# Kernel tuning notes

Measured on AMD Instinct MI355X. Metric: run time of the kernel, lower is better.

## Reference

```python
import jax, jax.numpy as jnp
import numpy as np

N = 20000      # nodes
E = 640000     # edges (avg degree 32)
F_X = 256      # node feature dim
F_E = 256      # edge feature dim
D = 2048       # hidden width
D_OUT = 512    # final Linear out_channels
EPS = 1e-5     # torch LayerNorm default eps


def _glorot_like(k, fan_in, fan_out):
    # torch nn.Linear default: U(-1/sqrt(fan_in), 1/sqrt(fan_in))
    lim = (1.0 / fan_in) ** 0.5
    return jax.random.uniform(k, (fan_in, fan_out), minval=-lim, maxval=lim, dtype=jnp.float32)


def setup_inputs() -> dict:
    key = jax.random.key(0)
    ks = jax.random.split(key, 8)
    return {
        "x": jax.random.normal(ks[0], (N, F_X), dtype=jnp.float32),
        "edge_index": jax.random.randint(ks[1], (2, E), 0, N),
        "edge_attr": jax.random.normal(ks[2], (E, F_E), dtype=jnp.float32),
        # u = (u, nb, eb) in the original; unused by this setup (no conv1d/GraphNorm)
        "u_counts": jnp.array([N], dtype=jnp.int32),
        "nb": jnp.zeros((N,), dtype=jnp.int32),
        "eb": jnp.zeros((E,), dtype=jnp.int32),
        # learned params per setup
        "W1": _glorot_like(ks[3], F_X + F_E, D), "b1": jnp.zeros((D,), jnp.float32),
        "W3": _glorot_like(ks[4], D, D),         "b3": jnp.zeros((D,), jnp.float32),
        "ln_g": jnp.ones((D,), jnp.float32),      "ln_b": jnp.zeros((D,), jnp.float32),
        "W6": _glorot_like(ks[5], D + F_X + F_E, D), "b6": jnp.zeros((D,), jnp.float32),
        "W8": _glorot_like(ks[6], D, D_OUT),      "b8": jnp.zeros((D_OUT,), jnp.float32),
    }


def reference(x, edge_index, edge_attr, u_counts, nb, eb,
              W1, b1, W3, b3, ln_g, ln_b, W6, b6, W8, b8):
    # scatter_mean(edge_attr, col, dim=0, dim_size=N)
    col = edge_index[1]
    seg_sum = jax.ops.segment_sum(edge_attr, col, num_segments=N)           # [N, F_E]
    cnt = jax.ops.segment_sum(jnp.ones((edge_attr.shape[0],), edge_attr.dtype),
                              col, num_segments=N)                           # [N]
    agg = seg_sum / jnp.maximum(cnt, 1.0)[:, None]                           # mean; 0 for empty slots

    h0 = jnp.concatenate([agg, x], axis=1)                                   # [N, F_E+F_X]
    # layer 1-2: Linear -> ReLU
    h2 = jax.nn.relu(h0 @ W1 + b1)                                           # [N, D]
    # layer 3-4: Linear -> ReLU
    h4 = jax.nn.relu(h2 @ W3 + b3)                                           # [N, D]
    # layer 5: LayerNorm (affine)
    mu = jnp.mean(h4, axis=-1, keepdims=True)
    var = jnp.var(h4, axis=-1, keepdims=True)
    h5 = (h4 - mu) * jax.lax.rsqrt(var + EPS) * ln_g + ln_b
    # layer 6-7: Linear over concat(h5, merge_in) -> ReLU  (skip connection)
    h7 = jax.nn.relu(jnp.concatenate([h5, h0], axis=1) @ W6 + b6)            # [N, D]
    # layer 8: Linear -> out[-1]
    return h7 @ W8 + b8                                                      # [N, D_OUT]
```

## Files before the change

### kernel.cpp

```cpp
#include <hip/hip_runtime.h>

typedef unsigned short ushort_t;
typedef __attribute__((ext_vector_type(4))) float f32x4;
typedef __attribute__((ext_vector_type(8))) __bf16 bf16x8;
typedef __attribute__((ext_vector_type(8))) unsigned short u16x8;
typedef __attribute__((ext_vector_type(4))) unsigned short u16x4;

__device__ __forceinline__ unsigned short f2bf(float f) {
  union { float f; unsigned int u; } v; v.f = f;
  unsigned int u = v.u;
  u += 0x7fffu + ((u >> 16) & 1u);
  return (unsigned short)(u >> 16);
}

__device__ __forceinline__ float bf2f(unsigned short h) {
  union { unsigned int u; float f; } v; v.u = ((unsigned int)h) << 16;
  return v.f;
}

__device__ __forceinline__ void gload16(ushort_t* lds, const ushort_t* g) {
  __builtin_amdgcn_global_load_lds(
      (const __attribute__((address_space(1))) unsigned int*)g,
      (__attribute__((address_space(3))) unsigned int*)lds, 16, 0, 0);
}

__global__ __launch_bounds__(256)
void transpose_w(const float* __restrict__ in, ushort_t* __restrict__ out, int R, int C) {
  __shared__ float tile[32][33];
  const int t = threadIdx.x;
  const int tx = t & 31, ty = t >> 5;
  const int r0 = blockIdx.x * 32, c0 = blockIdx.y * 32;
#pragma unroll
  for (int i = 0; i < 4; ++i)
    tile[ty + 8 * i][tx] = in[(size_t)(r0 + ty + 8 * i) * C + c0 + tx];
  __syncthreads();
#pragma unroll
  for (int i = 0; i < 4; ++i)
    out[(size_t)(c0 + ty + 8 * i) * R + r0 + tx] = f2bf(tile[tx][ty + 8 * i]);
}

__global__ __launch_bounds__(256)
void count_edges(const int* __restrict__ col, int* __restrict__ cnt, int E) {
  int i = blockIdx.x * 256 + threadIdx.x;
  if (i < E) atomicAdd(&cnt[col[i]], 1);
}

__global__ __launch_bounds__(1024)
void prefix_kernel(const int* __restrict__ cnt, int* __restrict__ start,
                   int* __restrict__ cursor, int N) {
  const int t = threadIdx.x;
  const int chunk = (N + 1023) >> 10;
  const int base = t * chunk;
  int s = 0;
  for (int j = 0; j < chunk; ++j) {
    int i = base + j;
    s += (i < N) ? cnt[i] : 0;
  }
  const int lane = t & 63, wv = t >> 6;
  int scan = s;
#pragma unroll
  for (int o = 1; o < 64; o <<= 1) {
    int up = __shfl_up(scan, o);
    if (lane >= o) scan += up;
  }
  __shared__ int wsum[16];
  if (lane == 63) wsum[wv] = scan;
  __syncthreads();
  if (t == 0) {
    int acc = 0;
#pragma unroll
    for (int i2 = 0; i2 < 16; ++i2) { int v = wsum[i2]; wsum[i2] = acc; acc += v; }
  }
  __syncthreads();
  int run = wsum[wv] + (scan - s);
  for (int j = 0; j < chunk; ++j) {
    int i = base + j;
    if (i < N) {
      start[i] = run; cursor[i] = run;
      run += cnt[i];
    }
  }
}

__global__ __launch_bounds__(256)
void fill_csr(const int* __restrict__ col, int* __restrict__ cursor,
              int* __restrict__ eids, int E) {
  int i = blockIdx.x * 256 + threadIdx.x;
  if (i < E) {
    int p = atomicAdd(&cursor[col[i]], 1);
    eids[p] = i;
  }
}

__global__ __launch_bounds__(256)
void gather_mean(const float* __restrict__ eattr, const int* __restrict__ start,
                 const int* __restrict__ deg, const int* __restrict__ eids,
                 const float* __restrict__ x, ushort_t* __restrict__ hcat, int N) {
  const int row = blockIdx.x;
  const int t = threadIdx.x;
  const int w = t >> 6, l = t & 63;
  const int s = start[row], d = deg[row];
  const float4* ea4 = (const float4*)eattr;
  float4 sum = make_float4(0.f, 0.f, 0.f, 0.f);
  for (int i = w; i < d; i += 4) {
    int e = eids[s + i];
    float4 v = ea4[(size_t)e * 64 + l];
    sum.x += v.x; sum.y += v.y; sum.z += v.z; sum.w += v.w;
  }
  __shared__ float4 part[4][64];
  part[w][l] = sum;
  __syncthreads();
  hcat[(size_t)row * 2560 + 2304 + t] = f2bf(x[(size_t)row * 256 + t]);
  if (w == 0) {
    float4 a = part[0][l], b = part[1][l], c = part[2][l], dd = part[3][l];
    const float inv = 1.f / fmaxf((float)d, 1.f);
    u16x4 o;
    o[0] = f2bf((a.x + b.x + c.x + dd.x) * inv);
    o[1] = f2bf((a.y + b.y + c.y + dd.y) * inv);
    o[2] = f2bf((a.z + b.z + c.z + dd.z) * inv);
    o[3] = f2bf((a.w + b.w + c.w + dd.w) * inv);
    *(u16x4*)(hcat + (size_t)row * 2560 + 2048 + l * 4) = o;
  }
}

__global__ __launch_bounds__(256)
void ln_kernel(ushort_t* __restrict__ hcat, const float* __restrict__ g,
               const float* __restrict__ b) {
  const int row = blockIdx.x;
  const int t = threadIdx.x;
  ushort_t* p = hcat + (size_t)row * 2560 + t * 8;
  u16x8 raw = *(const u16x8*)p;
  float vv[8];
#pragma unroll
  for (int j = 0; j < 8; ++j) vv[j] = bf2f(raw[j]);
  float s = 0.f, ss = 0.f;
#pragma unroll
  for (int j = 0; j < 8; ++j) { s += vv[j]; ss += vv[j] * vv[j]; }
#pragma unroll
  for (int o = 32; o > 0; o >>= 1) {
    s += __shfl_xor(s, o);
    ss += __shfl_xor(ss, o);
  }
  __shared__ float red[8];
  int w = t >> 6, l = t & 63;
  if (l == 0) { red[w] = s; red[4 + w] = ss; }
  __syncthreads();
  s = red[0] + red[1] + red[2] + red[3];
  ss = red[4] + red[5] + red[6] + red[7];
  const float mu = s * (1.f / 2048.f);
  const float var = ss * (1.f / 2048.f) - mu * mu;
  const float rs = rsqrtf(var + 1e-5f);
  float4 g0 = *(const float4*)(g + t * 8);
  float4 g1 = *(const float4*)(g + t * 8 + 4);
  float4 b0 = *(const float4*)(b + t * 8);
  float4 b1 = *(const float4*)(b + t * 8 + 4);
  float gg[8] = {g0.x, g0.y, g0.z, g0.w, g1.x, g1.y, g1.z, g1.w};
  float bb[8] = {b0.x, b0.y, b0.z, b0.w, b1.x, b1.y, b1.z, b1.w};
  u16x8 o8;
#pragma unroll
  for (int j = 0; j < 8; ++j) o8[j] = f2bf((vv[j] - mu) * rs * gg[j] + bb[j]);
  *(u16x8*)p = o8;
}


__device__ __forceinline__ void read_a4(bf16x8 (&dst)[4][2], const char* sb, int bufoff,
                                        int aoff, int slot0, int slot1, int g) {
#pragma unroll
  for (int m = 0; m < 4; ++m) {
    const char* p = sb + bufoff + aoff + (g * 4 + m) * 2048;
    dst[m][0] = *(const bf16x8*)(p + slot0);
    dst[m][1] = *(const bf16x8*)(p + slot1);
  }
}

__device__ __forceinline__ void read_b2(bf16x8 (&dst)[2][2], const char* sb, int bufoff,
                                        int boff, int slot0, int slot1, int g) {
#pragma unroll
  for (int n = 0; n < 2; ++n) {
    const char* p = sb + bufoff + boff + (g * 2 + n) * 2048;
    dst[n][0] = *(const bf16x8*)(p + slot0);
    dst[n][1] = *(const bf16x8*)(p + slot1);
  }
}

__device__ __forceinline__ void mfma_q(f32x4 (&acc)[8][4], const bf16x8 (&a)[4][2],
                                       const bf16x8 (&b)[2][2], int mg, int ng) {
#pragma unroll
  for (int m = 0; m < 4; ++m)
#pragma unroll
    for (int n = 0; n < 2; ++n)
#pragma unroll
      for (int kk = 0; kk < 2; ++kk)
        acc[mg * 4 + m][ng * 2 + n] = __builtin_amdgcn_mfma_f32_16x16x32_bf16(
            a[m][kk], b[n][kk], acc[mg * 4 + m][ng * 2 + n], 0, 0, 0);
}

#define SBAR() do { __builtin_amdgcn_sched_barrier(0); \
                    __builtin_amdgcn_s_barrier(); \
                    __builtin_amdgcn_sched_barrier(0); } while (0)

template <int RELU, int OUTBF>
__global__ __launch_bounds__(512, 2)
void gemm256(const ushort_t* __restrict__ A, int lda,
             const ushort_t* __restrict__ Bt,
             const float* __restrict__ bias,
             void* __restrict__ Cout, int ldc, int M, int K) {
  __shared__ __align__(16) ushort_t smem[65536];
  char* sb = (char*)smem;
  const int t = threadIdx.x;

  const int nct = gridDim.x;
  const int nwg = nct * gridDim.y;
  const int flat = blockIdx.y * nct + blockIdx.x;
  const int xcd = flat & 7, loc = flat >> 3;
  const int q = nwg >> 3, r = nwg & 7;
  const int swz = (xcd < r ? xcd * (q + 1) : r * (q + 1) + (xcd - r) * q) + loc;
  const int row0 = (swz / nct) * 256;
  const int col0 = (swz % nct) * 256;

  const int wid = t >> 6, l = t & 63;
  const int wr = wid >> 2, wc = wid & 3;
  const int lr = l & 15, lk = l >> 4;

  const int srow = t >> 3;
  const int scol = ((t & 7) ^ ((t >> 3) & 7)) << 3;
  const ushort_t* pa[2][2];
  const ushort_t* pb[2][2];
#pragma unroll
  for (int h = 0; h < 2; ++h)
#pragma unroll
    for (int L = 0; L < 2; ++L) {
      int ra = row0 + h * 128 + L * 64 + srow;
      if (ra > M - 1) ra = M - 1;
      pa[h][L] = A + (size_t)ra * lda + scol;
      pb[h][L] = Bt + (size_t)(col0 + h * 128 + L * 64 + srow) * K + scol;
    }
  const int tb = t * 16;

  const int slot0 = ((lk ^ (lr & 7)) << 4);
  const int slot1 = (((4 + lk) ^ (lr & 7)) << 4);
  const int aoff = (wr * 128 + lr) * 128;
  const int boff = 32768 + (wc * 64 + lr) * 128;

  f32x4 acc[8][4] = {};
  bf16x8 af[4][2], af2[4][2], bf[2][2], bf2[2][2];

  const int nk = K >> 6;

  {
    gload16((ushort_t*)(sb + 0 + tb), pa[0][0]);
    gload16((ushort_t*)(sb + 8192 + tb), pa[0][1]);
    gload16((ushort_t*)(sb + 16384 + tb), pa[1][0]);
    gload16((ushort_t*)(sb + 24576 + tb), pa[1][1]);
    gload16((ushort_t*)(sb + 32768 + tb), pb[0][0]);
    gload16((ushort_t*)(sb + 40960 + tb), pb[0][1]);
    gload16((ushort_t*)(sb + 49152 + tb), pb[1][0]);
    gload16((ushort_t*)(sb + 57344 + tb), pb[1][1]);
    const int k1 = (nk > 1) ? 1 : 0;
    gload16((ushort_t*)(sb + 65536 + 32768 + tb), pb[0][0] + (k1 << 6));
    gload16((ushort_t*)(sb + 65536 + 40960 + tb), pb[0][1] + (k1 << 6));
    gload16((ushort_t*)(sb + 65536 + 0 + tb), pa[0][0] + (k1 << 6));
    gload16((ushort_t*)(sb + 65536 + 8192 + tb), pa[0][1] + (k1 << 6));
  }
  asm volatile("s_waitcnt vmcnt(4)" ::: "memory");
  SBAR();

  for (int k = 0; k < nk; ++k) {
    const int cur = (k & 1) << 16, nxt = cur ^ 65536;
    const int kc1 = ((k + 1 < nk) ? k + 1 : nk - 1) << 6;
    const int kc2 = ((k + 2 < nk) ? k + 2 : nk - 1) << 6;

    read_a4(af, sb, cur, aoff, slot0, slot1, 0);
    read_b2(bf, sb, cur, boff, slot0, slot1, 0);
    gload16((ushort_t*)(sb + nxt + 16384 + tb), pa[1][0] + kc1);
    gload16((ushort_t*)(sb + nxt + 24576 + tb), pa[1][1] + kc1);
    SBAR();
    __builtin_amdgcn_s_setprio(1);
    mfma_q(acc, af, bf, 0, 0);
    __builtin_amdgcn_s_setprio(0);
    SBAR();

    read_b2(bf2, sb, cur, boff, slot0, slot1, 1);
    gload16((ushort_t*)(sb + nxt + 49152 + tb), pb[1][0] + kc1);
    gload16((ushort_t*)(sb + nxt + 57344 + tb), pb[1][1] + kc1);
    SBAR();
    __builtin_amdgcn_s_setprio(1);
    mfma_q(acc, af, bf2, 0, 1);
    __builtin_amdgcn_s_setprio(0);
    SBAR();

    read_a4(af2, sb, cur, aoff, slot0, slot1, 1);
    gload16((ushort_t*)(sb + cur + 32768 + tb), pb[0][0] + kc2);
    gload16((ushort_t*)(sb + cur + 40960 + tb), pb[0][1] + kc2);
    SBAR();
    __builtin_amdgcn_s_setprio(1);
    mfma_q(acc, af2, bf, 1, 0);
    __builtin_amdgcn_s_setprio(0);
    SBAR();

    gload16((ushort_t*)(sb + cur + 0 + tb), pa[0][0] + kc2);
    gload16((ushort_t*)(sb + cur + 8192 + tb), pa[0][1] + kc2);
    asm volatile("s_waitcnt vmcnt(4)" ::: "memory");
    SBAR();
    __builtin_amdgcn_s_setprio(1);
    mfma_q(acc, af2, bf2, 1, 1);
    __builtin_amdgcn_s_setprio(0);
    SBAR();
  }

#pragma unroll
  for (int nj = 0; nj < 4; ++nj) {
    const int ocol = col0 + wc * 64 + nj * 16 + lr;
    const float bv = bias[ocol];
#pragma unroll
    for (int mi = 0; mi < 8; ++mi) {
      const int orow = row0 + wr * 128 + mi * 16 + lk * 4;
      f32x4 v = acc[mi][nj];
#pragma unroll
      for (int r2 = 0; r2 < 4; ++r2) {
        if (orow + r2 < M) {
          float o = v[r2] + bv;
          if (RELU) o = fmaxf(o, 0.f);
          if (OUTBF)
            ((ushort_t*)Cout)[(size_t)(orow + r2) * ldc + ocol] = f2bf(o);
          else
            ((float*)Cout)[(size_t)(orow + r2) * ldc + ocol] = o;
        }
      }
    }
  }
}

extern "C" void kernel_launch(void* const* d_in, const int* in_sizes, int n_in,
                              void* d_out, int out_size, void* d_ws, size_t ws_size,
                              hipStream_t stream) {
  (void)n_in; (void)out_size; (void)ws_size;
  const float* x     = (const float*)d_in[0];
  const int*   eidx  = (const int*)d_in[1];
  const float* eattr = (const float*)d_in[2];
  const float* W1 = (const float*)d_in[6];
  const float* b1 = (const float*)d_in[7];
  const float* W3 = (const float*)d_in[8];
  const float* b3 = (const float*)d_in[9];
  const float* lng = (const float*)d_in[10];
  const float* lnb = (const float*)d_in[11];
  const float* W6 = (const float*)d_in[12];
  const float* b6 = (const float*)d_in[13];
  const float* W8 = (const float*)d_in[14];
  const float* b8 = (const float*)d_in[15];

  const int N = in_sizes[0] / 256;
  const int E = in_sizes[2] / 256;
  const int* col = eidx + E;

  char* ws = (char*)d_ws;
  size_t off = 0;
  ushort_t* hcat = (ushort_t*)(ws + off);  off += (size_t)N * 2560 * 2;
  ushort_t* h2   = (ushort_t*)(ws + off);  off += (size_t)N * 2048 * 2;
  ushort_t* W1t = (ushort_t*)(ws + off);   off += (size_t)2048 * 512 * 2;
  ushort_t* W3t = (ushort_t*)(ws + off);   off += (size_t)2048 * 2048 * 2;
  ushort_t* W6t = (ushort_t*)(ws + off);   off += (size_t)2048 * 2560 * 2;
  ushort_t* W8t = (ushort_t*)(ws + off);   off += (size_t)512 * 2048 * 2;
  int* deg    = (int*)(ws + off);  off += (size_t)N * 4;
  int* startp = (int*)(ws + off);  off += (size_t)N * 4;
  int* cursor = (int*)(ws + off);  off += (size_t)N * 4;
  int* eids   = (int*)(ws + off);  off += (size_t)E * 4;

  hipMemsetAsync(deg, 0, (size_t)N * 4, stream);

  transpose_w<<<dim3(512 / 32, 2048 / 32), 256, 0, stream>>>(W1, W1t, 512, 2048);
  transpose_w<<<dim3(2048 / 32, 2048 / 32), 256, 0, stream>>>(W3, W3t, 2048, 2048);
  transpose_w<<<dim3(2560 / 32, 2048 / 32), 256, 0, stream>>>(W6, W6t, 2560, 2048);
  transpose_w<<<dim3(2048 / 32, 512 / 32), 256, 0, stream>>>(W8, W8t, 2048, 512);

  count_edges<<<(E + 255) / 256, 256, 0, stream>>>(col, deg, E);
  prefix_kernel<<<1, 1024, 0, stream>>>(deg, startp, cursor, N);
  fill_csr<<<(E + 255) / 256, 256, 0, stream>>>(col, cursor, eids, E);
  gather_mean<<<N, 256, 0, stream>>>(eattr, startp, deg, eids, x, hcat, N);

  const int Mt256 = (N + 255) / 256;
  gemm256<1, 1><<<dim3(8, Mt256), 512, 0, stream>>>(hcat + 2048, 2560, W1t, b1, h2, 2048, N, 512);
  gemm256<1, 1><<<dim3(8, Mt256), 512, 0, stream>>>(h2, 2048, W3t, b3, hcat, 2560, N, 2048);
  ln_kernel<<<N, 256, 0, stream>>>(hcat, lng, lnb);
  gemm256<1, 1><<<dim3(8, Mt256), 512, 0, stream>>>(hcat, 2560, W6t, b6, h2, 2048, N, 2560);
  gemm256<0, 0><<<dim3(2, Mt256), 512, 0, stream>>>(h2, 2048, W8t, b8, (float*)d_out, 512, N, 2048);
}
```

Measured before the change: 932.7 us.

## Replace 256x256 GEMM tile with 128x256 tile and triple-buffered K=32 pipeline

Swaps the 256x256-tile GEMM, which used K=64 steps, two LDS buffers and 128KB of shared memory, for a 128x256 tile that walks K in steps of 32. The new loop uses three LDS stages of 24KB each, with prefetch two steps ahead. Launch bounds go to 4 blocks per CU and the grid doubles along M. The goal is higher occupancy and better tail balance over 20000 rows. In exchange, arithmetic intensity per tile drops and B-tile reuse falls, so global and LDS traffic per FLOP rise.

```diff
diff --git a/kernel.cpp b/kernel.cpp
--- a/kernel.cpp
+++ b/kernel.cpp
@@ -163,49 +163,17 @@
 }
 
 
-__device__ __forceinline__ void read_a4(bf16x8 (&dst)[4][2], const char* sb, int bufoff,
-                                        int aoff, int slot0, int slot1, int g) {
-#pragma unroll
-  for (int m = 0; m < 4; ++m) {
-    const char* p = sb + bufoff + aoff + (g * 4 + m) * 2048;
-    dst[m][0] = *(const bf16x8*)(p + slot0);
-    dst[m][1] = *(const bf16x8*)(p + slot1);
-  }
-}
-
-__device__ __forceinline__ void read_b2(bf16x8 (&dst)[2][2], const char* sb, int bufoff,
-                                        int boff, int slot0, int slot1, int g) {
-#pragma unroll
-  for (int n = 0; n < 2; ++n) {
-    const char* p = sb + bufoff + boff + (g * 2 + n) * 2048;
-    dst[n][0] = *(const bf16x8*)(p + slot0);
-    dst[n][1] = *(const bf16x8*)(p + slot1);
-  }
-}
-
-__device__ __forceinline__ void mfma_q(f32x4 (&acc)[8][4], const bf16x8 (&a)[4][2],
-                                       const bf16x8 (&b)[2][2], int mg, int ng) {
-#pragma unroll
-  for (int m = 0; m < 4; ++m)
-#pragma unroll
-    for (int n = 0; n < 2; ++n)
-#pragma unroll
-      for (int kk = 0; kk < 2; ++kk)
-        acc[mg * 4 + m][ng * 2 + n] = __builtin_amdgcn_mfma_f32_16x16x32_bf16(
-            a[m][kk], b[n][kk], acc[mg * 4 + m][ng * 2 + n], 0, 0, 0);
-}
-
 #define SBAR() do { __builtin_amdgcn_sched_barrier(0); \
                     __builtin_amdgcn_s_barrier(); \
                     __builtin_amdgcn_sched_barrier(0); } while (0)
 
 template <int RELU, int OUTBF>
-__global__ __launch_bounds__(512, 2)
-void gemm256(const ushort_t* __restrict__ A, int lda,
+__global__ __launch_bounds__(512, 4)
+void gemm128(const ushort_t* __restrict__ A, int lda,
              const ushort_t* __restrict__ Bt,
              const float* __restrict__ bias,
              void* __restrict__ Cout, int ldc, int M, int K) {
-  __shared__ __align__(16) ushort_t smem[65536];
+  __shared__ __align__(16) ushort_t smem[36864];
   char* sb = (char*)smem;
   const int t = threadIdx.x;
 
@@ -215,97 +183,81 @@
   const int xcd = flat & 7, loc = flat >> 3;
   const int q = nwg >> 3, r = nwg & 7;
   const int swz = (xcd < r ? xcd * (q + 1) : r * (q + 1) + (xcd - r) * q) + loc;
-  const int row0 = (swz / nct) * 256;
+  const int row0 = (swz / nct) * 128;
   const int col0 = (swz % nct) * 256;
 
   const int wid = t >> 6, l = t & 63;
   const int wr = wid >> 2, wc = wid & 3;
   const int lr = l & 15, lk = l >> 4;
 
-  const int srow = t >> 3;
-  const int scol = ((t & 7) ^ ((t >> 3) & 7)) << 3;
-  const ushort_t* pa[2][2];
-  const ushort_t* pb[2][2];
-#pragma unroll
-  for (int h = 0; h < 2; ++h)
-#pragma unroll
-    for (int L = 0; L < 2; ++L) {
-      int ra = row0 + h * 128 + L * 64 + srow;
-      if (ra > M - 1) ra = M - 1;
-      pa[h][L] = A + (size_t)ra * lda + scol;
-      pb[h][L] = Bt + (size_t)(col0 + h * 128 + L * 64 + srow) * K + scol;
-    }
+  const int srow = t >> 2;
+  const int scol = ((t & 3) ^ ((t >> 2) & 3)) << 3;
+  int ar = row0 + srow; if (ar > M - 1) ar = M - 1;
+  const ushort_t* pa  = A + (size_t)ar * lda + scol;
+  const ushort_t* pb0 = Bt + (size_t)(col0 + srow) * K + scol;
+  const ushort_t* pb1 = pb0 + (size_t)128 * K;
   const int tb = t * 16;
 
-  const int slot0 = ((lk ^ (lr & 7)) << 4);
-  const int slot1 = (((4 + lk) ^ (lr & 7)) << 4);
-  const int aoff = (wr * 128 + lr) * 128;
-  const int boff = 32768 + (wc * 64 + lr) * 128;
-
-  f32x4 acc[8][4] = {};
-  bf16x8 af[4][2], af2[4][2], bf[2][2], bf2[2][2];
-
-  const int nk = K >> 6;
+  const int sx = ((lk ^ (lr & 3)) << 4);
+  const int arow = (wr * 64 + lr) * 64 + sx;
+  const int brow = 8192 + (wc * 64 + lr) * 64 + sx;
+
+  f32x4 acc[4][4] = {};
+  bf16x8 a[4], b01[2], b23[2];
+
+  const int nk = K >> 5;
 
   {
-    gload16((ushort_t*)(sb + 0 + tb), pa[0][0]);
-    gload16((ushort_t*)(sb + 8192 + tb), pa[0][1]);
-    gload16((ushort_t*)(sb + 16384 + tb), pa[1][0]);
-    gload16((ushort_t*)(sb + 24576 + tb), pa[1][1]);
-    gload16((ushort_t*)(sb + 32768 + tb), pb[0][0]);
-    gload16((ushort_t*)(sb + 40960 + tb), pb[0][1]);
-    gload16((ushort_t*)(sb + 49152 + tb), pb[1][0]);
-    gload16((ushort_t*)(sb + 57344 + tb), pb[1][1]);
-    const int k1 = (nk > 1) ? 1 : 0;
-    gload16((ushort_t*)(sb + 65536 + 32768 + tb), pb[0][0] + (k1 << 6));
-    gload16((ushort_t*)(sb + 65536 + 40960 + tb), pb[0][1] + (k1 << 6));
-    gload16((ushort_t*)(sb + 65536 + 0 + tb), pa[0][0] + (k1 << 6));
-    gload16((ushort_t*)(sb + 65536 + 8192 + tb), pa[0][1] + (k1 << 6));
-  }
-  asm volatile("s_waitcnt vmcnt(4)" ::: "memory");
+    const int k1 = (nk > 1) ? 32 : 0;
+    gload16((ushort_t*)(sb + 8192 + tb), pb0);
+    gload16((ushort_t*)(sb + 16384 + tb), pb1);
+    gload16((ushort_t*)(sb + 0 + tb), pa);
+    gload16((ushort_t*)(sb + 24576 + 8192 + tb), pb0 + k1);
+    gload16((ushort_t*)(sb + 24576 + 16384 + tb), pb1 + k1);
+    gload16((ushort_t*)(sb + 24576 + 0 + tb), pa + k1);
+  }
+  asm volatile("s_waitcnt vmcnt(3)" ::: "memory");
   SBAR();
 
+  int cO = 0, sO = 49152;
   for (int k = 0; k < nk; ++k) {
-    const int cur = (k & 1) << 16, nxt = cur ^ 65536;
-    const int kc1 = ((k + 1 < nk) ? k + 1 : nk - 1) << 6;
-    const int kc2 = ((k + 2 < nk) ? k + 2 : nk - 1) << 6;
-
-    read_a4(af, sb, cur, aoff, slot0, slot1, 0);
-    read_b2(bf, sb, cur, boff, slot0, slot1, 0);
-    gload16((ushort_t*)(sb + nxt + 16384 + tb), pa[1][0] + kc1);
-    gload16((ushort_t*)(sb + nxt + 24576 + tb), pa[1][1] + kc1);
+    const int kc2 = ((k + 2 < nk) ? k + 2 : nk - 1) << 5;
+
+#pragma unroll
+    for (int m = 0; m < 4; ++m)
+      a[m] = *(const bf16x8*)(sb + cO + arow + m * 1024);
+#pragma unroll
+    for (int n = 0; n < 2; ++n)
+      b01[n] = *(const bf16x8*)(sb + cO + brow + n * 1024);
+    gload16((ushort_t*)(sb + sO + 8192 + tb), pb0 + kc2);
+    gload16((ushort_t*)(sb + sO + 16384 + tb), pb1 + kc2);
     SBAR();
     __builtin_amdgcn_s_setprio(1);
-    mfma_q(acc, af, bf, 0, 0);
+#pragma unroll
+    for (int m = 0; m < 4; ++m)
+#pragma unroll
+      for (int n = 0; n < 2; ++n)
+        acc[m][n] = __builtin_amdgcn_mfma_f32_16x16x32_bf16(a[m], b01[n], acc[m][n], 0, 0, 0);
     __builtin_amdgcn_s_setprio(0);
     SBAR();
 
-    read_b2(bf2, sb, cur, boff, slot0, slot1, 1);
-    gload16((ushort_t*)(sb + nxt + 49152 + tb), pb[1][0] + kc1);
-    gload16((ushort_t*)(sb + nxt + 57344 + tb), pb[1][1] + kc1);
+#pragma unroll
+    for (int n = 0; n < 2; ++n)
+      b23[n] = *(const bf16x8*)(sb + cO + brow + (2 + n) * 1024);
+    gload16((ushort_t*)(sb + sO + 0 + tb), pa + kc2);
     SBAR();
     __builtin_amdgcn_s_setprio(1);
-    mfma_q(acc, af, bf2, 0, 1);
+#pragma unroll
+    for (int m = 0; m < 4; ++m)
+#pragma unroll
+      for (int n = 0; n < 2; ++n)
+        acc[m][2 + n] = __builtin_amdgcn_mfma_f32_16x16x32_bf16(a[m], b23[n], acc[m][2 + n], 0, 0, 0);
     __builtin_amdgcn_s_setprio(0);
+    asm volatile("s_waitcnt vmcnt(3)" ::: "memory");
     SBAR();
 
-    read_a4(af2, sb, cur, aoff, slot0, slot1, 1);
-    gload16((ushort_t*)(sb + cur + 32768 + tb), pb[0][0] + kc2);
-    gload16((ushort_t*)(sb + cur + 40960 + tb), pb[0][1] + kc2);
-    SBAR();
-    __builtin_amdgcn_s_setprio(1);
-    mfma_q(acc, af2, bf, 1, 0);
-    __builtin_amdgcn_s_setprio(0);
-    SBAR();
-
-    gload16((ushort_t*)(sb + cur + 0 + tb), pa[0][0] + kc2);
-    gload16((ushort_t*)(sb + cur + 8192 + tb), pa[0][1] + kc2);
-    asm volatile("s_waitcnt vmcnt(4)" ::: "memory");
-    SBAR();
-    __builtin_amdgcn_s_setprio(1);
-    mfma_q(acc, af2, bf2, 1, 1);
-    __builtin_amdgcn_s_setprio(0);
-    SBAR();
+    cO = (cO == 49152) ? 0 : cO + 24576;
+    sO = (sO == 49152) ? 0 : sO + 24576;
   }
 
 #pragma unroll
@@ -313,8 +265,8 @@
     const int ocol = col0 + wc * 64 + nj * 16 + lr;
     const float bv = bias[ocol];
 #pragma unroll
-    for (int mi = 0; mi < 8; ++mi) {
-      const int orow = row0 + wr * 128 + mi * 16 + lk * 4;
+    for (int mi = 0; mi < 4; ++mi) {
+      const int orow = row0 + wr * 64 + mi * 16 + lk * 4;
       f32x4 v = acc[mi][nj];
 #pragma unroll
       for (int r2 = 0; r2 < 4; ++r2) {
@@ -378,10 +330,10 @@
   fill_csr<<<(E + 255) / 256, 256, 0, stream>>>(col, cursor, eids, E);
   gather_mean<<<N, 256, 0, stream>>>(eattr, startp, deg, eids, x, hcat, N);
 
-  const int Mt256 = (N + 255) / 256;
-  gemm256<1, 1><<<dim3(8, Mt256), 512, 0, stream>>>(hcat + 2048, 2560, W1t, b1, h2, 2048, N, 512);
-  gemm256<1, 1><<<dim3(8, Mt256), 512, 0, stream>>>(h2, 2048, W3t, b3, hcat, 2560, N, 2048);
+  const int Mt = (N + 127) / 128;
+  gemm128<1, 1><<<dim3(8, Mt), 512, 0, stream>>>(hcat + 2048, 2560, W1t, b1, h2, 2048, N, 512);
+  gemm128<1, 1><<<dim3(8, Mt), 512, 0, stream>>>(h2, 2048, W3t, b3, hcat, 2560, N, 2048);
   ln_kernel<<<N, 256, 0, stream>>>(hcat, lng, lnb);
-  gemm256<1, 1><<<dim3(8, Mt256), 512, 0, stream>>>(hcat, 2560, W6t, b6, h2, 2048, N, 2560);
-  gemm256<0, 0><<<dim3(2, Mt256), 512, 0, stream>>>(h2, 2048, W8t, b8, (float*)d_out, 512, N, 2048);
-}
+  gemm128<1, 1><<<dim3(8, Mt), 512, 0, stream>>>(hcat, 2560, W6t, b6, h2, 2048, N, 2560);
+  gemm128<0, 0><<<dim3(2, Mt), 512, 0, stream>>>(h2, 2048, W8t, b8, (float*)d_out, 512, N, 2048);
+}
```

Result: faster. 882.4 us (-5.4%).
